# Optimization experiments

Measured on AMD Instinct MI355X. Metric: run time of the kernel, lower is better.

Reference implementation:

```python
import jax, jax.numpy as jnp
import numpy as np

# Room-class id -> type code: ids 0..6 are 'separate' (living_room, kitchen, bedroom,
# missing, balcony, corridor, dining_room) -> code 0; ids 7,8 are 'flexible'
# (bathroom, laundry_room) -> code 1; id 9 is 'affiliated' (closet) -> code 2.
N_SEPARATE = 7
N_FLEXIBLE = 2


def setup_inputs() -> dict:
    key = jax.random.key(0)
    k1, k2 = jax.random.split(key)
    b, n, h, w = 32, 64, 128, 128
    masks = jax.random.normal(k1, (b, n, h, w), dtype=jnp.float32)
    nodes = jax.random.randint(k2, (n,), 0, N_SEPARATE + N_FLEXIBLE + 1, dtype=jnp.int64)
    return {"masks": masks, "nodes": nodes}


def _node_type(nodes):
    # 0 = separate, 1 = flexible, 2 = affiliated
    return jnp.where(nodes < N_SEPARATE, 0, jnp.where(nodes < N_SEPARATE + N_FLEXIBLE, 1, 2))


def reference(masks, nodes):
    b, n, h, w = masks.shape
    m = jnp.clip((masks + 1.0) / 2.0, 0.0, None).reshape(b, n, h * w)  # (b,n,hw)

    # Pairwise overlap Gram matrix and per-node mass sums
    gram = jnp.einsum("bik,bjk->bij", m, m)          # (b,n,n)  sum(mi*mj)
    s = m.sum(axis=-1)                                # (b,n)
    min_s = jnp.minimum(s[:, :, None], s[:, None, :]) # (b,n,n)
    cr = (gram / min_s).mean(axis=0)                  # (n,n) mean over batch

    # Static per-pair beta / skip logic from node types
    t = _node_type(nodes)                             # (n,)
    ti, tj = t[:, None], t[None, :]
    has_f = (ti == 1) | (tj == 1)
    has_a = (ti == 2) | (tj == 2)
    include = ~(has_f & ~has_a)                       # skip 'fs' and 'ff'
    beta = ((ti == 2) ^ (tj == 2)).astype(cr.dtype)   # 1 for 'as'/'af', 0 for 'ss'/'aa'

    triu = jnp.triu(jnp.ones((n, n), dtype=bool), k=1)
    wgt = (include & triu).astype(cr.dtype)
    loss = jnp.sum(jnp.abs(beta - cr) * wgt) / jnp.sum(wgt)
    return loss
```

## Files before the change

kernel.cpp:

```cpp
#include <hip/hip_runtime.h>
#include <cstdint>
#include <cstddef>

static constexpr int HW_ = 16384;
static constexpr int NB_ = 32;
static constexpr int NN_ = 64;
static constexpr int BK_ = 64;

typedef short bfrag  __attribute__((ext_vector_type(8)));
typedef float f32x4  __attribute__((ext_vector_type(4)));

__device__ __forceinline__ unsigned short f2bf_rne(float x) {
    unsigned u = __builtin_bit_cast(unsigned, x);
    return (unsigned short)((u + 0x7FFFu + ((u >> 16) & 1u)) >> 16);
}

__device__ __forceinline__ int swz(int row, int k) {
    int byte = (row << 7) + (k << 1);
    byte ^= (row & 7) << 4;
    return byte >> 1;
}

__global__ __launch_bounds__(256) void gram_kernel(const float* __restrict__ masks,
                                                   float* __restrict__ gram_part,
                                                   float* __restrict__ s_part,
                                                   int NC, int KC) {
    __shared__ __align__(16) unsigned short lds[2][NN_ * BK_];
    const int bx = blockIdx.x;
    const int b  = bx / NC;
    const int c  = bx - b * NC;
    const int t  = threadIdx.x;
    const int l  = t & 63;
    const int w  = t >> 6;
    const int lrow = t >> 4;
    const int lk4  = t & 15;
    const float* mb = masks + (size_t)b * (NN_ * HW_) + (size_t)c * KC;
    const int NT = KC / BK_;

    f32x4 acc[4];
#pragma unroll
    for (int cb = 0; cb < 4; ++cb) acc[cb] = (f32x4){0.f, 0.f, 0.f, 0.f};
    float sreg[4] = {0.f, 0.f, 0.f, 0.f};
    float4 ld[4];

    auto stage_load = [&](int tt) {
        const float* src = mb + tt * BK_ + lk4 * 4;
#pragma unroll
        for (int p = 0; p < 4; ++p)
            ld[p] = *reinterpret_cast<const float4*>(src + (size_t)(lrow + 16 * p) * HW_);
    };
    auto stage_write = [&](unsigned short* buf) {
#pragma unroll
        for (int p = 0; p < 4; ++p) {
            const float m0 = fmaxf(0.f, (ld[p].x + 1.f) * 0.5f);
            const float m1 = fmaxf(0.f, (ld[p].y + 1.f) * 0.5f);
            const float m2 = fmaxf(0.f, (ld[p].z + 1.f) * 0.5f);
            const float m3 = fmaxf(0.f, (ld[p].w + 1.f) * 0.5f);
            sreg[p] += (m0 + m1) + (m2 + m3);
            const ushort4 pk = make_ushort4(f2bf_rne(m0), f2bf_rne(m1),
                                            f2bf_rne(m2), f2bf_rne(m3));
            *reinterpret_cast<ushort4*>(&buf[swz(lrow + 16 * p, lk4 * 4)]) = pk;
        }
    };
    auto compute = [&](const unsigned short* buf) {
#pragma unroll
        for (int ks = 0; ks < BK_; ks += 32) {
            const int kb = ks + ((l >> 4) << 3);
            const bfrag a = *reinterpret_cast<const bfrag*>(&buf[swz((w << 4) + (l & 15), kb)]);
#pragma unroll
            for (int cb = 0; cb < 4; ++cb) {
                const bfrag bb = *reinterpret_cast<const bfrag*>(&buf[swz((cb << 4) + (l & 15), kb)]);
                acc[cb] = __builtin_amdgcn_mfma_f32_16x16x32_bf16(a, bb, acc[cb], 0, 0, 0);
            }
        }
    };

    stage_load(0);
    stage_write(lds[0]);
    __syncthreads();
    for (int tt = 0; tt < NT; ++tt) {
        const int cur = tt & 1;
        const bool more = (tt + 1 < NT);
        if (more) stage_load(tt + 1);
        compute(lds[cur]);
        if (more) stage_write(lds[cur ^ 1]);
        __syncthreads();
    }

    float* gp = gram_part + (size_t)(c * NB_ + b) * (NN_ * NN_);
#pragma unroll
    for (int cb = 0; cb < 4; ++cb)
#pragma unroll
        for (int r = 0; r < 4; ++r) {
            const int i = (w << 4) + ((l >> 4) << 2) + r;
            const int j = (cb << 4) + (l & 15);
            gp[i * NN_ + j] = acc[cb][r];
        }
#pragma unroll
    for (int p = 0; p < 4; ++p) {
        float v = sreg[p];
        v += __shfl_xor(v, 1, 64);
        v += __shfl_xor(v, 2, 64);
        v += __shfl_xor(v, 4, 64);
        v += __shfl_xor(v, 8, 64);
        if ((l & 15) == 0)
            s_part[(size_t)c * (NB_ * NN_) + b * NN_ + (lrow + 16 * p)] = v;
    }
}

__global__ void s_reduce_kernel(const float* __restrict__ s_part,
                                float* __restrict__ s_full, int NC) {
    const int b = blockIdx.x;
    const int t = threadIdx.x;
    float v = 0.f;
    for (int c = 0; c < NC; ++c)
        v += s_part[(size_t)c * (NB_ * NN_) + b * NN_ + t];
    s_full[b * NN_ + t] = v;
}

__global__ void cr_weight_kernel(const float* __restrict__ gram_part,
                                 const float* __restrict__ s_full,
                                 float* __restrict__ wq, int NC) {
    const int b  = blockIdx.x;
    const int ij = blockIdx.y * 256 + threadIdx.x;
    float g = 0.f;
#pragma unroll 8
    for (int c = 0; c < NC; ++c)
        g += gram_part[(size_t)(c * NB_ + b) * (NN_ * NN_) + ij];
    const int i = ij >> 6, j = ij & 63;
    const float si = s_full[b * NN_ + i];
    const float sj = s_full[b * NN_ + j];
    wq[(size_t)b * (NN_ * NN_) + ij] = g / fminf(si, sj);
}

__global__ void loss2_kernel(const float* __restrict__ wq,
                             const int* __restrict__ nodes,
                             float* __restrict__ num_part,
                             float* __restrict__ den_part) {
    __shared__ float red[8];
    const int ij = blockIdx.x * 256 + threadIdx.x;
    float acc = 0.f;
#pragma unroll
    for (int b = 0; b < NB_; ++b)
        acc += wq[(size_t)b * (NN_ * NN_) + ij];
    const float cr = acc * (1.0f / NB_);

    const int i = ij >> 6, j = ij & 63;
    const int ni = nodes[i];
    const int nj = nodes[j];
    const int ti = (ni < 7) ? 0 : ((ni < 9) ? 1 : 2);
    const int tj = (nj < 7) ? 0 : ((nj < 9) ? 1 : 2);
    const bool has_f = (ti == 1) || (tj == 1);
    const bool has_a = (ti == 2) || (tj == 2);
    const bool include = !(has_f && !has_a);
    const float beta = ((ti == 2) != (tj == 2)) ? 1.f : 0.f;
    const float wgt = (include && (j > i)) ? 1.f : 0.f;

    float num = wgt * fabsf(beta - cr);
    float den = wgt;
#pragma unroll
    for (int off = 32; off >= 1; off >>= 1) {
        num += __shfl_xor(num, off, 64);
        den += __shfl_xor(den, off, 64);
    }
    const int wave = threadIdx.x >> 6;
    const int lane = threadIdx.x & 63;
    if (lane == 0) { red[wave] = num; red[4 + wave] = den; }
    __syncthreads();
    if (threadIdx.x == 0) {
        num_part[blockIdx.x] = red[0] + red[1] + red[2] + red[3];
        den_part[blockIdx.x] = red[4] + red[5] + red[6] + red[7];
    }
}

__global__ void final_kernel(const float* __restrict__ num_part,
                             const float* __restrict__ den_part,
                             float* __restrict__ out) {
    const int t = threadIdx.x;
    float num = (t < 16) ? num_part[t] : 0.f;
    float den = (t < 16) ? den_part[t] : 0.f;
#pragma unroll
    for (int off = 32; off >= 1; off >>= 1) {
        num += __shfl_xor(num, off, 64);
        den += __shfl_xor(den, off, 64);
    }
    if (t == 0) out[0] = num / den;
}

extern "C" void kernel_launch(void* const* d_in, const int* in_sizes, int n_in,
                              void* d_out, int out_size, void* d_ws, size_t ws_size,
                              hipStream_t stream) {
    const float* masks = (const float*)d_in[0];
    const int* nodes = (const int*)d_in[1];
    float* out = (float*)d_out;

    const size_t ws_floats = ws_size / sizeof(float);
    int NC = 32;
    while (NC > 1) {
        const size_t need = (size_t)NC * NB_ * NN_ * NN_
                          + (size_t)NC * NB_ * NN_
                          + (size_t)NB_ * NN_
                          + (size_t)NB_ * NN_ * NN_
                          + 2 * 16;
        if (need <= ws_floats) break;
        NC >>= 1;
    }
    const int KC = HW_ / NC;

    float* gram_part = (float*)d_ws;
    float* s_part    = gram_part + (size_t)NC * NB_ * NN_ * NN_;
    float* s_full    = s_part    + (size_t)NC * NB_ * NN_;
    float* wq        = s_full    + (size_t)NB_ * NN_;
    float* num_part  = wq        + (size_t)NB_ * NN_ * NN_;
    float* den_part  = num_part  + 16;

    gram_kernel<<<NB_ * NC, 256, 0, stream>>>(masks, gram_part, s_part, NC, KC);
    s_reduce_kernel<<<NB_, 64, 0, stream>>>(s_part, s_full, NC);
    cr_weight_kernel<<<dim3(NB_, (NN_ * NN_) / 256), 256, 0, stream>>>(gram_part, s_full, wq, NC);
    loss2_kernel<<<(NN_ * NN_) / 256, 256, 0, stream>>>(wq, nodes, num_part, den_part);
    final_kernel<<<1, 64, 0, stream>>>(num_part, den_part, out);
}
```

Measured before the change: 45.59 us.

## Fuse reduction kernels, use last-block atomic finalize, halve K-split chunks

```diff
diff --git a/kernel.cpp b/kernel.cpp
--- a/kernel.cpp
+++ b/kernel.cpp
@@ -108,36 +108,35 @@
     }
 }
 
-__global__ void s_reduce_kernel(const float* __restrict__ s_part,
-                                float* __restrict__ s_full, int NC) {
+__global__ __launch_bounds__(256) void cr_weight_kernel(const float* __restrict__ gram_part,
+                                                        const float* __restrict__ s_part,
+                                                        float* __restrict__ wq, int NC) {
+    __shared__ float s_loc[NN_];
     const int b = blockIdx.x;
-    const int t = threadIdx.x;
-    float v = 0.f;
-    for (int c = 0; c < NC; ++c)
-        v += s_part[(size_t)c * (NB_ * NN_) + b * NN_ + t];
-    s_full[b * NN_ + t] = v;
-}
-
-__global__ void cr_weight_kernel(const float* __restrict__ gram_part,
-                                 const float* __restrict__ s_full,
-                                 float* __restrict__ wq, int NC) {
-    const int b  = blockIdx.x;
+    if (threadIdx.x < NN_) {
+        float v = 0.f;
+        for (int c = 0; c < NC; ++c)
+            v += s_part[(size_t)c * (NB_ * NN_) + b * NN_ + threadIdx.x];
+        s_loc[threadIdx.x] = v;
+    }
+    __syncthreads();
     const int ij = blockIdx.y * 256 + threadIdx.x;
     float g = 0.f;
 #pragma unroll 8
     for (int c = 0; c < NC; ++c)
         g += gram_part[(size_t)(c * NB_ + b) * (NN_ * NN_) + ij];
     const int i = ij >> 6, j = ij & 63;
-    const float si = s_full[b * NN_ + i];
-    const float sj = s_full[b * NN_ + j];
-    wq[(size_t)b * (NN_ * NN_) + ij] = g / fminf(si, sj);
-}
-
-__global__ void loss2_kernel(const float* __restrict__ wq,
-                             const int* __restrict__ nodes,
-                             float* __restrict__ num_part,
-                             float* __restrict__ den_part) {
+    wq[(size_t)b * (NN_ * NN_) + ij] = g / fminf(s_loc[i], s_loc[j]);
+}
+
+__global__ __launch_bounds__(256) void loss2_kernel(const float* __restrict__ wq,
+                                                    const int* __restrict__ nodes,
+                                                    float* __restrict__ num_part,
+                                                    float* __restrict__ den_part,
+                                                    unsigned int* __restrict__ counter,
+                                                    float* __restrict__ out) {
     __shared__ float red[8];
+    __shared__ int is_last;
     const int ij = blockIdx.x * 256 + threadIdx.x;
     float acc = 0.f;
 #pragma unroll
@@ -168,23 +167,29 @@
     if (lane == 0) { red[wave] = num; red[4 + wave] = den; }
     __syncthreads();
     if (threadIdx.x == 0) {
-        num_part[blockIdx.x] = red[0] + red[1] + red[2] + red[3];
-        den_part[blockIdx.x] = red[4] + red[5] + red[6] + red[7];
-    }
-}
-
-__global__ void final_kernel(const float* __restrict__ num_part,
-                             const float* __restrict__ den_part,
-                             float* __restrict__ out) {
-    const int t = threadIdx.x;
-    float num = (t < 16) ? num_part[t] : 0.f;
-    float den = (t < 16) ? den_part[t] : 0.f;
-#pragma unroll
-    for (int off = 32; off >= 1; off >>= 1) {
-        num += __shfl_xor(num, off, 64);
-        den += __shfl_xor(den, off, 64);
-    }
-    if (t == 0) out[0] = num / den;
+        const float bn = red[0] + red[1] + red[2] + red[3];
+        const float bd = red[4] + red[5] + red[6] + red[7];
+        __hip_atomic_store(&num_part[blockIdx.x], bn, __ATOMIC_RELAXED, __HIP_MEMORY_SCOPE_AGENT);
+        __hip_atomic_store(&den_part[blockIdx.x], bd, __ATOMIC_RELAXED, __HIP_MEMORY_SCOPE_AGENT);
+        const unsigned old = __hip_atomic_fetch_add(counter, 1u, __ATOMIC_ACQ_REL,
+                                                    __HIP_MEMORY_SCOPE_AGENT);
+        is_last = (old == (unsigned)(gridDim.x - 1));
+    }
+    __syncthreads();
+    if (is_last && threadIdx.x < 64) {
+        const int t = threadIdx.x;
+        float n16 = 0.f, d16 = 0.f;
+        if (t < 16) {
+            n16 = __hip_atomic_load(&num_part[t], __ATOMIC_RELAXED, __HIP_MEMORY_SCOPE_AGENT);
+            d16 = __hip_atomic_load(&den_part[t], __ATOMIC_RELAXED, __HIP_MEMORY_SCOPE_AGENT);
+        }
+#pragma unroll
+        for (int off = 8; off >= 1; off >>= 1) {
+            n16 += __shfl_xor(n16, off, 64);
+            d16 += __shfl_xor(d16, off, 64);
+        }
+        if (t == 0) out[0] = n16 / d16;
+    }
 }
 
 extern "C" void kernel_launch(void* const* d_in, const int* in_sizes, int n_in,
@@ -195,13 +200,12 @@
     float* out = (float*)d_out;
 
     const size_t ws_floats = ws_size / sizeof(float);
-    int NC = 32;
+    int NC = 16;
     while (NC > 1) {
         const size_t need = (size_t)NC * NB_ * NN_ * NN_
                           + (size_t)NC * NB_ * NN_
-                          + (size_t)NB_ * NN_
                           + (size_t)NB_ * NN_ * NN_
-                          + 2 * 16;
+                          + 2 * 16 + 4;
         if (need <= ws_floats) break;
         NC >>= 1;
     }
@@ -209,14 +213,13 @@
 
     float* gram_part = (float*)d_ws;
     float* s_part    = gram_part + (size_t)NC * NB_ * NN_ * NN_;
-    float* s_full    = s_part    + (size_t)NC * NB_ * NN_;
-    float* wq        = s_full    + (size_t)NB_ * NN_;
+    float* wq        = s_part    + (size_t)NC * NB_ * NN_;
     float* num_part  = wq        + (size_t)NB_ * NN_ * NN_;
     float* den_part  = num_part  + 16;
-
+    unsigned int* counter = (unsigned int*)(den_part + 16);
+
+    hipMemsetAsync(counter, 0, sizeof(unsigned int), stream);
     gram_kernel<<<NB_ * NC, 256, 0, stream>>>(masks, gram_part, s_part, NC, KC);
-    s_reduce_kernel<<<NB_, 64, 0, stream>>>(s_part, s_full, NC);
-    cr_weight_kernel<<<dim3(NB_, (NN_ * NN_) / 256), 256, 0, stream>>>(gram_part, s_full, wq, NC);
-    loss2_kernel<<<(NN_ * NN_) / 256, 256, 0, stream>>>(wq, nodes, num_part, den_part);
-    final_kernel<<<1, 64, 0, stream>>>(num_part, den_part, out);
-}
+    cr_weight_kernel<<<dim3(NB_, (NN_ * NN_) / 256), 256, 0, stream>>>(gram_part, s_part, wq, NC);
+    loss2_kernel<<<(NN_ * NN_) / 256, 256, 0, stream>>>(wq, nodes, num_part, den_part, counter, out);
+}
```

After: 42.40 us. 1.08x faster.
